# Kernel tuning notes

Measured on AMD Instinct MI355X. Metric: run time of the kernel, lower is better.

The kernel has to match this reference:

```python
import jax, jax.numpy as jnp
import numpy as np

IN_F, OUT_F = 1024, 1024
GRID_SIZE, SPLINE_ORDER = 5, 3
BATCH = 4096


def _make_grid():
    # grid_range = [-1, 1], h = 2 / grid_size
    h = 2.0 / GRID_SIZE
    g = jnp.arange(-SPLINE_ORDER, GRID_SIZE + SPLINE_ORDER + 1, dtype=jnp.float32) * h - 1.0
    return jnp.broadcast_to(g, (IN_F, g.shape[0]))  # [in, 12]


def setup_inputs() -> dict:
    key = jax.random.key(0)
    k1, k2, k3, k4 = jax.random.split(key, 4)
    x = jax.random.normal(k1, (BATCH, IN_F), dtype=jnp.float32) * 0.5
    base_weight = jax.random.normal(k2, (OUT_F, IN_F), dtype=jnp.float32) * (1.0 / np.sqrt(IN_F))
    # matches reset_parameters noise scale: (rand-0.5)*0.1/grid_size
    spline_weight = (jax.random.uniform(k3, (OUT_F, IN_F, GRID_SIZE + SPLINE_ORDER)) - 0.5) * (0.1 / GRID_SIZE)
    spline_scaler = jax.random.normal(k4, (OUT_F, IN_F), dtype=jnp.float32) * (1.0 / np.sqrt(IN_F))
    return {"x": x, "base_weight": base_weight, "spline_weight": spline_weight,
            "spline_scaler": spline_scaler, "grid": _make_grid()}


def _b_splines(x, grid):
    # x: [B, F], grid: [F, G]; returns [B, F, grid_size + spline_order]
    xe = x[..., None]  # [B, F, 1]
    bases = ((xe >= grid[:, :-1]) & (xe < grid[:, 1:])).astype(x.dtype)  # [B,F,G-1]
    for k in range(1, SPLINE_ORDER + 1):
        left = (xe - grid[:, : -(k + 1)]) / (grid[:, k:-1] - grid[:, : -(k + 1)])
        right = (grid[:, k + 1 :] - xe) / (grid[:, k + 1 :] - grid[:, 1:-k])
        bases = left * bases[:, :, :-1] + right * bases[:, :, 1:]
    return bases


def reference(x, base_weight, spline_weight, spline_scaler, grid):
    base_out = jax.nn.silu(x) @ base_weight.T  # [B, out]
    basis = _b_splines(x, grid)  # [B, in, 8]
    scaled_w = spline_weight * spline_scaler[..., None]  # [out, in, 8]
    spline_out = jnp.einsum('bfi,ofi->bo', basis, scaled_w)
    return base_out + spline_out
```

## Files before the change

kernel.cpp:

```cpp
#include <hip/hip_runtime.h>
#include <hip/hip_bf16.h>

#define IN_F   1024
#define OUT_F  1024
#define GS     5
#define SO     3
#define NB     (GS + SO)
#define NG     (GS + 2*SO + 1)
#define BATCH  4096
#define KC     (IN_F + IN_F * NB)
#define BM 256
#define BN 256
#define BK 64
#define SPLITK 4
#define KPART  (KC / SPLITK)
#define NT     (KPART / BK)

typedef __bf16 bf16x8 __attribute__((ext_vector_type(8)));
typedef float  f32x4  __attribute__((ext_vector_type(4)));

__device__ __forceinline__ void gload_lds16(const void* g, void* l) {
    __builtin_amdgcn_global_load_lds(
        (const __attribute__((address_space(1))) void*)g,
        (__attribute__((address_space(3))) void*)l,
        16, 0, 0);
}

#define WC_BLK 4608
#define A_BLK  18432

__global__ __launch_bounds__(256) void prep_all(const float* __restrict__ bw,
                                                const float* __restrict__ sw,
                                                const float* __restrict__ ss,
                                                const float* __restrict__ x,
                                                __bf16* __restrict__ W,
                                                __bf16* __restrict__ A) {
    if (blockIdx.x < WC_BLK) {
        const int t = blockIdx.x * 256 + threadIdx.x;
        const int NBASE = OUT_F * IN_F / 8;
        if (t < NBASE) {
            const int o  = t >> 7;
            const int c8 = (t & 127) * 8;
            const float4* sp = (const float4*)(bw + (size_t)o * IN_F + c8);
            float4 v0 = sp[0], v1 = sp[1];
            float v[8] = {v0.x, v0.y, v0.z, v0.w, v1.x, v1.y, v1.z, v1.w};
            bf16x8 ov;
#pragma unroll
            for (int j = 0; j < 8; ++j) ov[j] = (__bf16)v[j];
            *(bf16x8*)(W + (size_t)o * KC + c8) = ov;
        } else {
            const int u = t - NBASE;
            if (u >= OUT_F * IN_F) return;
            const int o = u >> 10, f = u & 1023;
            const float s = ss[(size_t)o * IN_F + f];
            const float4* sp = (const float4*)(sw + ((size_t)o * IN_F + f) * NB);
            float4 v0 = sp[0], v1 = sp[1];
            float v[8] = {v0.x, v0.y, v0.z, v0.w, v1.x, v1.y, v1.z, v1.w};
            bf16x8 ov;
#pragma unroll
            for (int j = 0; j < 8; ++j) ov[j] = (__bf16)(v[j] * s);
            *(bf16x8*)(W + (size_t)o * KC + IN_F + (size_t)f * NB) = ov;
        }
    } else {
        const int t = (blockIdx.x - WC_BLK) * 256 + threadIdx.x;
        const int NBASE = BATCH * IN_F / 8;
        if (t < NBASE) {
            const int b  = t >> 7;
            const int c8 = (t & 127) * 8;
            const float4* sp = (const float4*)(x + (size_t)b * IN_F + c8);
            float4 v0 = sp[0], v1 = sp[1];
            float v[8] = {v0.x, v0.y, v0.z, v0.w, v1.x, v1.y, v1.z, v1.w};
            bf16x8 ov;
#pragma unroll
            for (int j = 0; j < 8; ++j) {
                float xx = v[j];
                ov[j] = (__bf16)(xx / (1.0f + __expf(-xx)));
            }
            *(bf16x8*)(A + (size_t)b * KC + c8) = ov;
        } else {
            const int u = t - NBASE;
            if (u >= BATCH * IN_F) return;
            const int b = u >> 10, f = u & 1023;
            const float xv = x[(size_t)b * IN_F + f];
            const float h = 2.0f / GS;
            float gv[NG];
#pragma unroll
            for (int j = 0; j < NG; ++j) gv[j] = (float)(j - SO) * h - 1.0f;
            float bas[NB + SO];
#pragma unroll
            for (int j = 0; j < NB + SO; ++j)
                bas[j] = (xv >= gv[j] && xv < gv[j + 1]) ? 1.0f : 0.0f;
#pragma unroll
            for (int k = 1; k <= SO; ++k) {
                const float rk = 1.0f / ((float)k * h);
#pragma unroll
                for (int j = 0; j <= (NB + SO - 1) - k; ++j) {
                    float left  = (xv - gv[j]) * rk;
                    float right = (gv[j + k + 1] - xv) * rk;
                    bas[j] = left * bas[j] + right * bas[j + 1];
                }
            }
            bf16x8 ov;
#pragma unroll
            for (int i = 0; i < NB; ++i) ov[i] = (__bf16)bas[i];
            *(bf16x8*)(A + (size_t)b * KC + IN_F + (size_t)f * NB) = ov;
        }
    }
}

__global__ __launch_bounds__(256) void zero_out(float4* __restrict__ p, int n4) {
    const int i = blockIdx.x * 256 + threadIdx.x;
    if (i < n4) p[i] = float4{0.f, 0.f, 0.f, 0.f};
}

__global__ __launch_bounds__(256) void reduce_k(float4* __restrict__ C,
                                                const float4* __restrict__ P) {
    const size_t n4 = (size_t)BATCH * OUT_F / 4;
    for (size_t i = blockIdx.x * 256 + threadIdx.x; i < n4; i += 2048 * 256) {
        float4 c  = C[i];
        float4 p0 = P[i];
        float4 p1 = P[n4 + i];
        float4 p2 = P[2 * n4 + i];
        c.x += p0.x + p1.x + p2.x;
        c.y += p0.y + p1.y + p2.y;
        c.z += p0.z + p1.z + p2.z;
        c.w += p0.w + p1.w + p2.w;
        C[i] = c;
    }
}

#define MFMAQ(AF, BF, MI0, NI0)                                               \
    __builtin_amdgcn_s_setprio(1);                                            \
    _Pragma("unroll")                                                         \
    for (int kk_ = 0; kk_ < 2; ++kk_)                                         \
        _Pragma("unroll")                                                     \
        for (int i_ = 0; i_ < 4; ++i_)                                        \
            _Pragma("unroll")                                                 \
            for (int n_ = 0; n_ < 2; ++n_)                                    \
                acc[(MI0) + i_][(NI0) + n_] =                                 \
                    __builtin_amdgcn_mfma_f32_16x16x32_bf16(                  \
                        AF[i_][kk_], BF[n_][kk_],                             \
                        acc[(MI0) + i_][(NI0) + n_], 0, 0, 0);                \
    __builtin_amdgcn_s_setprio(0);

#define RD_A4(DST, LBUF, MI0)                                                 \
    _Pragma("unroll")                                                         \
    for (int i_ = 0; i_ < 4; ++i_) {                                          \
        DST[i_][0] = *(const bf16x8*)&(LBUF)[((MI0) + i_) * 1024 + aRow + slot0]; \
        DST[i_][1] = *(const bf16x8*)&(LBUF)[((MI0) + i_) * 1024 + aRow + slot1]; \
    }

#define RD_B2(DST, LBUF, NI0)                                                 \
    _Pragma("unroll")                                                         \
    for (int n_ = 0; n_ < 2; ++n_) {                                          \
        DST[n_][0] = *(const bf16x8*)&(LBUF)[bRow + ((NI0) + n_) * 1024 + slot0]; \
        DST[n_][1] = *(const bf16x8*)&(LBUF)[bRow + ((NI0) + n_) * 1024 + slot1]; \
    }

#define LGKM_FENCE(N)                                                         \
    asm volatile("s_waitcnt lgkmcnt(" #N ")" ::: "memory");                   \
    __builtin_amdgcn_sched_barrier(0)

template<bool ATOMIC>
__global__ __launch_bounds__(512, 2) void kan_gemm(const __bf16* __restrict__ A,
                                                   const __bf16* __restrict__ W,
                                                   float* __restrict__ C,
                                                   float* __restrict__ P) {
    __shared__ __bf16 sA[2][2][128 * BK];
    __shared__ __bf16 sB[2][2][128 * BK];

    const int tid  = threadIdx.x;
    const int gid  = blockIdx.x;
    const int work = (gid & 7) * 32 + (gid >> 3);
    const int ks = work >> 6;
    const int bn = (work >> 4) & 3;
    const int bm = work & 15;

    const int lane = tid & 63;
    const int wv   = tid >> 6;
    const int wm   = wv >> 2;
    const int wn   = wv & 3;
    const int lr   = lane & 15;
    const int hi   = lane >> 4;
    const int key  = lr & 7;

    const int slot0 = ((hi ^ key) << 3);
    const int slot1 = (((4 + hi) ^ key) << 3);
    const int aRow  = lr * 64;
    const int bRow  = ((wn & 1) * 64 + lr) * 64;

    const int srow = tid >> 3;
    const int scol = ((tid & 7) ^ (srow & 7)) << 3;

    const __bf16* gA = A + (size_t)(bm * BM) * KC + ks * KPART;
    const __bf16* gW = W + (size_t)(bn * BN) * KC + ks * KPART;

    f32x4 acc[8][4] = {};
    bf16x8 a0[4][2], a1[4][2], b01[2][2], b23[2][2];

    auto stageA = [&](int buf, int h, int kt) {
#pragma unroll
        for (int l = 0; l < 2; ++l)
            gload_lds16(gA + (size_t)(h * 128 + l * 64 + srow) * KC + kt * BK + scol,
                        &sA[buf][h][(l * 512 + tid) * 8]);
    };
    auto stageB = [&](int buf, int h, int kt) {
#pragma unroll
        for (int l = 0; l < 2; ++l)
            gload_lds16(gW + (size_t)(h * 128 + l * 64 + srow) * KC + kt * BK + scol,
                        &sB[buf][h][(l * 512 + tid) * 8]);
    };

    stageA(0, 0, 0); stageA(0, 1, 0); stageB(0, 0, 0); stageB(0, 1, 0);
    stageA(1, 0, 1); stageA(1, 1, 1); stageB(1, 0, 1);
    asm volatile("s_waitcnt vmcnt(6)\n\ts_barrier" ::: "memory");

    for (int kt = 0; kt < NT; ++kt) {
        const int b = kt & 1;
        const __bf16* LA = &sA[b][wm][0];
        const __bf16* LB = &sB[b][wn >> 1][0];

        RD_A4(a0, LA, 0);
        RD_B2(b01, LB, 0);
        __builtin_amdgcn_sched_barrier(0);

        RD_B2(b23, LB, 2);
        LGKM_FENCE(4);
        MFMAQ(a0, b01, 0, 0);

        RD_A4(a1, LA, 4);
        if (kt + 1 < NT) stageB(b ^ 1, 1, kt + 1);
        LGKM_FENCE(8);
        __builtin_amdgcn_s_barrier();
        MFMAQ(a0, b23, 0, 2);

        if (kt + 2 < NT) stageB(b, 0, kt + 2);
        LGKM_FENCE(0);
        __builtin_amdgcn_s_barrier();
        MFMAQ(a1, b01, 4, 0);

        if (kt + 2 < NT) { stageA(b, 0, kt + 2); stageA(b, 1, kt + 2); }
        MFMAQ(a1, b23, 4, 2);

        if (kt + 2 < NT)
            asm volatile("s_waitcnt vmcnt(6)\n\ts_barrier" ::: "memory");
        else if (kt + 1 < NT)
            asm volatile("s_waitcnt vmcnt(0)\n\ts_barrier" ::: "memory");
    }

    const int cr = hi * 4, cc = lane & 15;
    float* dst;
    if (ATOMIC) dst = C;
    else        dst = (ks == 0) ? C : P + (size_t)(ks - 1) * BATCH * OUT_F;
#pragma unroll
    for (int mi = 0; mi < 8; ++mi)
#pragma unroll
        for (int ni = 0; ni < 4; ++ni) {
            float* cp = dst + (size_t)(bm * BM + wm * 128 + mi * 16 + cr) * OUT_F
                            + bn * BN + wn * 64 + ni * 16 + cc;
#pragma unroll
            for (int r = 0; r < 4; ++r) {
                if (ATOMIC) unsafeAtomicAdd(cp + (size_t)r * OUT_F, acc[mi][ni][r]);
                else        cp[(size_t)r * OUT_F] = acc[mi][ni][r];
            }
        }
}

extern "C" void kernel_launch(void* const* d_in, const int* in_sizes, int n_in,
                              void* d_out, int out_size, void* d_ws, size_t ws_size,
                              hipStream_t stream) {
    const float* x    = (const float*)d_in[0];
    const float* bw   = (const float*)d_in[1];
    const float* sw   = (const float*)d_in[2];
    const float* ss   = (const float*)d_in[3];

    const size_t wc_bytes   = (size_t)OUT_F * KC * 2;
    const size_t a_bytes    = (size_t)BATCH * KC * 2;
    const size_t part_bytes = 3ull * BATCH * OUT_F * 4;
    if (ws_size < wc_bytes + a_bytes) return;

    __bf16* Wc = (__bf16*)d_ws;
    __bf16* A  = (__bf16*)((char*)d_ws + wc_bytes);
    float*  P  = (float*)((char*)d_ws + wc_bytes + a_bytes);

    prep_all<<<WC_BLK + A_BLK, 256, 0, stream>>>(bw, sw, ss, x, Wc, A);

    const int grid = (BATCH / BM) * (OUT_F / BN) * SPLITK;
    if (ws_size >= wc_bytes + a_bytes + part_bytes) {
        kan_gemm<false><<<grid, 512, 0, stream>>>(A, Wc, (float*)d_out, P);
        reduce_k<<<2048, 256, 0, stream>>>((float4*)d_out, (const float4*)P);
    } else {
        const int n4 = BATCH * OUT_F / 4;
        zero_out<<<n4 / 256, 256, 0, stream>>>((float4*)d_out, n4);
        kan_gemm<true><<<grid, 512, 0, stream>>>(A, Wc, (float*)d_out, P);
    }
}
```

Before: 113.9 us.

## Fuse split-K reduction into GEMM via per-tile completion counters

Removes the separate reduce_k launch. Each GEMM block increments an atomic counter for its output tile, and the last of the four split-K blocks to arrive sums the partial buffers into C. The counters are zeroed by an extra block in the prep kernel. This saves a kernel launch and a full pass over the output. In exchange, the final reduction is serialized onto one block per tile with uncoalesced per-lane strided accesses, and correctness depends on acq_rel memory ordering between blocks.

```diff
diff --git a/kernel.cpp b/kernel.cpp
--- a/kernel.cpp
+++ b/kernel.cpp
@@ -34,7 +34,12 @@
                                                 const float* __restrict__ ss,
                                                 const float* __restrict__ x,
                                                 __bf16* __restrict__ W,
-                                                __bf16* __restrict__ A) {
+                                                __bf16* __restrict__ A,
+                                                int* __restrict__ cnt) {
+    if (blockIdx.x == WC_BLK + A_BLK) {
+        if (threadIdx.x < 64) cnt[threadIdx.x] = 0;
+        return;
+    }
     if (blockIdx.x < WC_BLK) {
         const int t = blockIdx.x * 256 + threadIdx.x;
         const int NBASE = OUT_F * IN_F / 8;
@@ -111,22 +116,6 @@
 __global__ __launch_bounds__(256) void zero_out(float4* __restrict__ p, int n4) {
     const int i = blockIdx.x * 256 + threadIdx.x;
     if (i < n4) p[i] = float4{0.f, 0.f, 0.f, 0.f};
-}
-
-__global__ __launch_bounds__(256) void reduce_k(float4* __restrict__ C,
-                                                const float4* __restrict__ P) {
-    const size_t n4 = (size_t)BATCH * OUT_F / 4;
-    for (size_t i = blockIdx.x * 256 + threadIdx.x; i < n4; i += 2048 * 256) {
-        float4 c  = C[i];
-        float4 p0 = P[i];
-        float4 p1 = P[n4 + i];
-        float4 p2 = P[2 * n4 + i];
-        c.x += p0.x + p1.x + p2.x;
-        c.y += p0.y + p1.y + p2.y;
-        c.z += p0.z + p1.z + p2.z;
-        c.w += p0.w + p1.w + p2.w;
-        C[i] = c;
-    }
 }
 
 #define MFMAQ(AF, BF, MI0, NI0)                                               \
@@ -165,9 +154,11 @@
 __global__ __launch_bounds__(512, 2) void kan_gemm(const __bf16* __restrict__ A,
                                                    const __bf16* __restrict__ W,
                                                    float* __restrict__ C,
-                                                   float* __restrict__ P) {
+                                                   float* __restrict__ P,
+                                                   int* __restrict__ cnt) {
     __shared__ __bf16 sA[2][2][128 * BK];
     __shared__ __bf16 sB[2][2][128 * BK];
+    __shared__ int lastFlag;
 
     const int tid  = threadIdx.x;
     const int gid  = blockIdx.x;
@@ -264,6 +255,32 @@
                 else        cp[(size_t)r * OUT_F] = acc[mi][ni][r];
             }
         }
+
+    if (!ATOMIC) {
+        __syncthreads();
+        if (tid == 0) {
+            int old = __hip_atomic_fetch_add(&cnt[bm * 4 + bn], 1,
+                        __ATOMIC_ACQ_REL, __HIP_MEMORY_SCOPE_AGENT);
+            lastFlag = (old == 3);
+        }
+        __syncthreads();
+        if (lastFlag) {
+            const size_t n1 = (size_t)BATCH * OUT_F;
+#pragma unroll
+            for (int mi = 0; mi < 8; ++mi)
+#pragma unroll
+                for (int ni = 0; ni < 4; ++ni) {
+                    const size_t off =
+                        (size_t)(bm * BM + wm * 128 + mi * 16 + cr) * OUT_F
+                        + bn * BN + wn * 64 + ni * 16 + cc;
+#pragma unroll
+                    for (int r = 0; r < 4; ++r) {
+                        const size_t o = off + (size_t)r * OUT_F;
+                        C[o] = C[o] + P[o] + P[n1 + o] + P[2 * n1 + o];
+                    }
+                }
+        }
+    }
 }
 
 extern "C" void kernel_launch(void* const* d_in, const int* in_sizes, int n_in,
@@ -277,21 +294,22 @@
     const size_t wc_bytes   = (size_t)OUT_F * KC * 2;
     const size_t a_bytes    = (size_t)BATCH * KC * 2;
     const size_t part_bytes = 3ull * BATCH * OUT_F * 4;
+    const size_t cnt_bytes  = 256;
     if (ws_size < wc_bytes + a_bytes) return;
 
-    __bf16* Wc = (__bf16*)d_ws;
-    __bf16* A  = (__bf16*)((char*)d_ws + wc_bytes);
-    float*  P  = (float*)((char*)d_ws + wc_bytes + a_bytes);
-
-    prep_all<<<WC_BLK + A_BLK, 256, 0, stream>>>(bw, sw, ss, x, Wc, A);
+    __bf16* Wc  = (__bf16*)d_ws;
+    __bf16* A   = (__bf16*)((char*)d_ws + wc_bytes);
+    float*  P   = (float*)((char*)d_ws + wc_bytes + a_bytes);
+    int*    cnt = (int*)((char*)d_ws + wc_bytes + a_bytes + part_bytes);
+
+    prep_all<<<WC_BLK + A_BLK + 1, 256, 0, stream>>>(bw, sw, ss, x, Wc, A, cnt);
 
     const int grid = (BATCH / BM) * (OUT_F / BN) * SPLITK;
-    if (ws_size >= wc_bytes + a_bytes + part_bytes) {
-        kan_gemm<false><<<grid, 512, 0, stream>>>(A, Wc, (float*)d_out, P);
-        reduce_k<<<2048, 256, 0, stream>>>((float4*)d_out, (const float4*)P);
+    if (ws_size >= wc_bytes + a_bytes + part_bytes + cnt_bytes) {
+        kan_gemm<false><<<grid, 512, 0, stream>>>(A, Wc, (float*)d_out, P, cnt);
     } else {
         const int n4 = BATCH * OUT_F / 4;
         zero_out<<<n4 / 256, 256, 0, stream>>>((float4*)d_out, n4);
-        kan_gemm<true><<<grid, 512, 0, stream>>>(A, Wc, (float*)d_out, P);
-    }
-}
+        kan_gemm<true><<<grid, 512, 0, stream>>>(A, Wc, (float*)d_out, P, cnt);
+    }
+}
```

New measurement: 133.0 us. +16.8%, slower.
